# Performance work log

Hardware: AMD Instinct MI355X
Metric: run time of the kernel (lower is better)

Reference implementation:

```python
import jax, jax.numpy as jnp
import numpy as np
import math

EPS = 1.1920929e-07  # torch F.rms_norm default eps = fp32 machine epsilon


def rms_norm(x):
    # normalize over last dim, no learned weight (matches F.rms_norm(x, (d,)))
    var = jnp.mean(jnp.square(x), axis=-1, keepdims=True)
    return x * jax.lax.rsqrt(var + EPS)


def rotary(x, cos, sin):
    # x: (B, T, H, D); cos/sin: (T, D) -> broadcast over B, H
    d2 = x.shape[-1] // 2
    x1, x2 = x[..., :d2], x[..., d2:]
    rot = jnp.concatenate([-x2, x1], axis=-1)  # rotate_half
    c = cos[None, :, None, :]
    s = sin[None, :, None, :]
    return x * c + rot * s


def setup_inputs() -> dict:
    key = jax.random.key(0)
    ks = jax.random.split(key, 5)
    B, T, C, H = 2, 2048, 1024, 16
    D = C // H
    x = jax.random.normal(ks[0], (B, T, C), dtype=jnp.float32)
    # real RoPE tables (theta=10000), duplicated across the two halves
    inv_freq = 1.0 / (10000.0 ** (np.arange(0, D, 2, dtype=np.float32) / D))
    pos = np.arange(T, dtype=np.float32)
    freqs = np.outer(pos, inv_freq)            # (T, D/2)
    emb = np.concatenate([freqs, freqs], -1)   # (T, D)
    cos = jnp.asarray(np.cos(emb), dtype=jnp.float32)
    sin = jnp.asarray(np.sin(emb), dtype=jnp.float32)
    sc_in = 1.0 / math.sqrt(C)
    W_attn = jax.random.normal(ks[1], (C, 3 * C), dtype=jnp.float32) * sc_in
    b_attn = jax.random.normal(ks[2], (3 * C,), dtype=jnp.float32) * 0.02
    W_proj = jax.random.normal(ks[3], (C, C), dtype=jnp.float32) * sc_in
    b_proj = jax.random.normal(ks[4], (C,), dtype=jnp.float32) * 0.02
    return {"x": x, "cos": cos, "sin": sin, "W_attn": W_attn, "b_attn": b_attn,
            "W_proj": W_proj, "b_proj": b_proj}


def reference(x, cos, sin, W_attn, b_attn, W_proj, b_proj):
    B, T, C = x.shape
    H = 16
    D = C // H
    qkv = x @ W_attn + b_attn                         # (B, T, 3C)
    qkv = qkv.reshape(B, T, 3, H, D)                  # 'b t (a h d) -> ...'
    q, k, v = qkv[:, :, 0], qkv[:, :, 1], qkv[:, :, 2]  # (B, T, H, D)
    q, k = rms_norm(q), rms_norm(k)
    q = rotary(q, cos, sin)
    k = rotary(k, cos, sin)
    # causal SDPA, scale = 1/sqrt(D)
    scale = 1.0 / math.sqrt(D)
    scores = jnp.einsum('bthd,bshd->bhts', q, k) * scale  # (B, H, T, T)
    causal = jnp.tril(jnp.ones((T, T), dtype=bool))
    scores = jnp.where(causal[None, None], scores, jnp.finfo(scores.dtype).min)
    attn = jax.nn.softmax(scores, axis=-1)
    y = jnp.einsum('bhts,bshd->bthd', attn, v)            # (B, T, H, D)
    y = y.reshape(B, T, C)
    return y @ W_proj + b_proj
```

## Files before the change

kernel.cpp:

```cpp
#include <hip/hip_runtime.h>
#include <math.h>

#define EPSV 1.1920929e-07f

typedef __attribute__((ext_vector_type(8))) short short8;
typedef __attribute__((ext_vector_type(4))) float f32x4;

__device__ __forceinline__ float bf2f(unsigned short u) {
    union { unsigned int i; float f; } c; c.i = ((unsigned int)u) << 16; return c.f;
}
__device__ __forceinline__ unsigned short f2bf(float f) {
    union { float f; unsigned int i; } c; c.f = f;
    unsigned int r = c.i + 0x7FFFu + ((c.i >> 16) & 1u);
    return (unsigned short)(r >> 16);
}
__device__ __forceinline__ unsigned int pack_bf16_ru(float a, float b) {
    union { float f; unsigned int i; } ca, cb; ca.f = a; cb.f = b;
    return __builtin_amdgcn_perm(cb.i + 0x8000u, ca.i + 0x8000u, 0x07060302u);
}
__device__ __forceinline__ void async_lds16(const unsigned short* g, unsigned short* l) {
    __builtin_amdgcn_global_load_lds(
        (const __attribute__((address_space(1))) unsigned int*)g,
        (__attribute__((address_space(3))) unsigned int*)l, 16, 0, 0);
}

__global__ __launch_bounds__(256) void prep_cast_transpose(
    const float* __restrict__ x, unsigned short* __restrict__ xb, int nCast,
    const float* __restrict__ Wa, unsigned short* __restrict__ Wat,
    const float* __restrict__ Wp, unsigned short* __restrict__ Wpt,
    const float* __restrict__ cosp, const float* __restrict__ sinp,
    float2* __restrict__ cs, int castBlocks)
{
    __shared__ float tile[32][33];
    const int bxg = blockIdx.x;
    if (bxg < castBlocks) {
        const int i = (bxg * 256 + threadIdx.x) * 4;
        if (i >= nCast) return;
        const float4 v = *(const float4*)&x[i];
        ushort4 o;
        o.x = f2bf(v.x); o.y = f2bf(v.y); o.z = f2bf(v.z); o.w = f2bf(v.w);
        *(ushort4*)&xb[i] = o;
        return;
    }
    if (bxg >= castBlocks + 4096) {
        const int i = (bxg - castBlocks - 4096) * 256 + threadIdx.x;
        const int tp = i >> 5, dp = i & 31;
        cs[i] = make_float2(cosp[tp * 64 + dp], sinp[tp * 64 + dp]);
        return;
    }
    const int r0 = bxg - castBlocks;
    int bx = r0 & 127;
    const int by = r0 >> 7;
    const float* W; unsigned short* Wt; int N;
    if (bx < 96) { W = Wa; Wt = Wat; N = 3072; }
    else         { W = Wp; Wt = Wpt; N = 1024; bx -= 96; }
    const int n0 = bx * 32, k0 = by * 32;
    const int r = threadIdx.x >> 3, c4 = (threadIdx.x & 7) * 4;
    const float4 v = *(const float4*)&W[(size_t)(k0 + r) * N + n0 + c4];
    tile[r][c4 + 0] = v.x; tile[r][c4 + 1] = v.y;
    tile[r][c4 + 2] = v.z; tile[r][c4 + 3] = v.w;
    __syncthreads();
    ushort4 o;
    o.x = f2bf(tile[c4 + 0][r]); o.y = f2bf(tile[c4 + 1][r]);
    o.z = f2bf(tile[c4 + 2][r]); o.w = f2bf(tile[c4 + 3][r]);
    *(ushort4*)&Wt[(size_t)(n0 + r) * 1024 + k0 + c4] = o;
}

__global__ __launch_bounds__(256) void gemm_qkv(
    const unsigned short* __restrict__ A,
    const unsigned short* __restrict__ Bt,
    const float* __restrict__ bias,
    unsigned short* __restrict__ qkv,
    unsigned short* __restrict__ vt,
    const float2* __restrict__ cs,
    int M, int K, int T)
{
    const int N = 3072;
    __shared__ __align__(16) unsigned short smem[17408];
    unsigned short* As0 = smem;
    unsigned short* As1 = smem + 4096;
    unsigned short* Bs0 = smem + 8192;
    unsigned short* Bs1 = smem + 12288;

    const int t    = threadIdx.x;
    const int lane = t & 63;
    const int wv   = t >> 6;
    const int wrow = (wv >> 1) * 64;
    const int wcol = (wv & 1) * 64;
    const int m0 = blockIdx.y * 128;
    const int n0 = blockIdx.x * 128;
    const int col  = lane & 15;
    const int quad = lane >> 4;

    const int srow = (wv << 5) + (lane >> 2);
    const int scol = (lane & 3) << 3;
    const unsigned short* a00 = A  + (size_t)(m0 + srow) * K + scol;
    const unsigned short* a10 = a00 + (size_t)16 * K;
    const unsigned short* a01 = a00 + 32;
    const unsigned short* a11 = a10 + 32;
    const unsigned short* b00 = Bt + (size_t)(n0 + srow) * K + scol;
    const unsigned short* b10 = b00 + (size_t)16 * K;
    const unsigned short* b01 = b00 + 32;
    const unsigned short* b11 = b10 + 32;
    unsigned short* al0 = &As0[srow * 32 + scol];
    unsigned short* al1 = &As0[(srow + 16) * 32 + scol];
    unsigned short* al2 = &As1[srow * 32 + scol];
    unsigned short* al3 = &As1[(srow + 16) * 32 + scol];
    unsigned short* bl0 = &Bs0[srow * 32 + scol];
    unsigned short* bl1 = &Bs0[(srow + 16) * 32 + scol];
    unsigned short* bl2 = &Bs1[srow * 32 + scol];
    unsigned short* bl3 = &Bs1[(srow + 16) * 32 + scol];

    f32x4 acc[4][4];
    #pragma unroll
    for (int i = 0; i < 4; ++i)
        #pragma unroll
        for (int j = 0; j < 4; ++j)
            acc[i][j] = (f32x4){0.f, 0.f, 0.f, 0.f};

    for (int k0 = 0; k0 < K; k0 += 64) {
        async_lds16(a00, al0);
        async_lds16(a10, al1);
        async_lds16(a01, al2);
        async_lds16(a11, al3);
        async_lds16(b00, bl0);
        async_lds16(b10, bl1);
        async_lds16(b01, bl2);
        async_lds16(b11, bl3);
        a00 += 64; a10 += 64; a01 += 64; a11 += 64;
        b00 += 64; b10 += 64; b01 += 64; b11 += 64;
        __syncthreads();
        short8 af[2][4], bf[2][4];
        #pragma unroll
        for (int mt = 0; mt < 4; ++mt) {
            af[0][mt] = *(const short8*)&As0[(wrow + mt * 16 + col) * 32 + (quad << 3)];
            af[1][mt] = *(const short8*)&As1[(wrow + mt * 16 + col) * 32 + (quad << 3)];
        }
        #pragma unroll
        for (int nt = 0; nt < 4; ++nt) {
            bf[0][nt] = *(const short8*)&Bs0[(wcol + nt * 16 + col) * 32 + (quad << 3)];
            bf[1][nt] = *(const short8*)&Bs1[(wcol + nt * 16 + col) * 32 + (quad << 3)];
        }
        #pragma unroll
        for (int ks = 0; ks < 2; ++ks)
            #pragma unroll
            for (int mt = 0; mt < 4; ++mt)
                #pragma unroll
                for (int nt = 0; nt < 4; ++nt)
                    acc[mt][nt] = __builtin_amdgcn_mfma_f32_16x16x32_bf16(
                        af[ks][mt], bf[ks][nt], acc[mt][nt], 0, 0, 0);
        __syncthreads();
    }

    #pragma unroll
    for (int nt = 0; nt < 4; ++nt) {
        const float bv = bias[n0 + wcol + nt * 16 + col];
        #pragma unroll
        for (int mt = 0; mt < 4; ++mt)
            #pragma unroll
            for (int r = 0; r < 4; ++r)
                acc[mt][nt][r] += bv;
    }

    const int b     = m0 / T;
    const int tpos0 = m0 - b * T;

    if (n0 < 2048) {
        const int n_lin = n0 + wcol;
        const float scale = (n_lin < 1024) ? 0.18033688011112042f : 1.0f;
        #pragma unroll
        for (int mt = 0; mt < 4; ++mt) {
            #pragma unroll
            for (int r = 0; r < 4; ++r) {
                float ss = acc[mt][0][r] * acc[mt][0][r]
                         + acc[mt][1][r] * acc[mt][1][r]
                         + acc[mt][2][r] * acc[mt][2][r]
                         + acc[mt][3][r] * acc[mt][3][r];
                ss += __shfl_xor(ss, 1, 64);
                ss += __shfl_xor(ss, 2, 64);
                ss += __shfl_xor(ss, 4, 64);
                ss += __shfl_xor(ss, 8, 64);
                const float rn = rsqrtf(ss * (1.0f / 64.0f) + EPSV) * scale;
                const int tpos = tpos0 + wrow + mt * 16 + (quad << 2) + r;
                const float2 c0 = cs[tpos * 32 + col];
                const float2 c1 = cs[tpos * 32 + 16 + col];
                const float o0 = (acc[mt][0][r] * c0.x - acc[mt][2][r] * c0.y) * rn;
                const float o1 = (acc[mt][1][r] * c1.x - acc[mt][3][r] * c1.y) * rn;
                const float o2 = (acc[mt][2][r] * c0.x + acc[mt][0][r] * c0.y) * rn;
                const float o3 = (acc[mt][3][r] * c1.x + acc[mt][1][r] * c1.y) * rn;
                const int m = m0 + wrow + mt * 16 + (quad << 2) + r;
                unsigned short* qr = qkv + (size_t)m * N + n_lin + col;
                qr[0]  = f2bf(o0);
                qr[16] = f2bf(o1);
                qr[32] = f2bf(o2);
                qr[48] = f2bf(o3);
            }
        }
    } else {
        unsigned short (*vtile)[136] = (unsigned short(*)[136])smem;
        __syncthreads();
        #pragma unroll
        for (int nt = 0; nt < 4; ++nt)
            #pragma unroll
            for (int mt = 0; mt < 4; ++mt)
                #pragma unroll
                for (int r = 0; r < 4; ++r)
                    vtile[wcol + nt * 16 + col][wrow + mt * 16 + (quad << 2) + r]
                        = f2bf(acc[mt][nt][r]);
        __syncthreads();
        const int td = t >> 4;
        const int mloc = (t & 15) << 3;
        const int h2base = (n0 - 2048) >> 6;
        #pragma unroll
        for (int i = 0; i < 8; ++i) {
            const int dl = td + i * 16;
            const short8 o = *(const short8*)&vtile[dl][mloc];
            const int h2 = h2base + (dl >> 6);
            const size_t row = ((size_t)(b * 16 + h2) << 6) + (dl & 63);
            *(short8*)&vt[row * T + tpos0 + mloc] = o;
        }
    }
}

__global__ __launch_bounds__(256) void gemm_bf16_n64(
    const unsigned short* __restrict__ A,
    const unsigned short* __restrict__ Bt,
    const float* __restrict__ bias,
    float* __restrict__ C,
    int M, int N, int K)
{
    __shared__ __align__(16) unsigned short smem[12288];
    const int t    = threadIdx.x;
    const int lane = t & 63;
    const int wv   = t >> 6;
    const int wrow = wv << 5;
    const int m0 = blockIdx.y * 128;
    const int n0 = blockIdx.x * 64;
    const int col  = lane & 15;
    const int quad = lane >> 4;

    const int srw = lane >> 2;
    const int sck = (lane & 3) << 3;
    const unsigned short* aP0 = A  + (size_t)(m0 + (wv << 4) + srw) * K + sck;
    const unsigned short* aP1 = aP0 + (size_t)64 * K;
    const unsigned short* bP0 = Bt + (size_t)(n0 + (wv << 4) + srw) * K + sck;
    const int stoff = (wv << 9) + (lane << 3);
    unsigned short* aD = smem + stoff;
    unsigned short* bD = smem + 8192 + stoff;

    f32x4 acc[2][4];
    #pragma unroll
    for (int i = 0; i < 2; ++i)
        #pragma unroll
        for (int j = 0; j < 4; ++j)
            acc[i][j] = (f32x4){0.f, 0.f, 0.f, 0.f};

    async_lds16(aP0, aD);  async_lds16(aP1, aD + 2048);
    async_lds16(bP0, bD);
    aP0 += 32; aP1 += 32; bP0 += 32;

    const int NK = K >> 5;
    for (int kt = 0; kt < NK; ++kt) {
        __syncthreads();
        if (kt + 1 < NK) {
            const int nbA = ((kt + 1) & 1) << 12;
            const int nbB = ((kt + 1) & 1) << 11;
            async_lds16(aP0, aD + nbA);  async_lds16(aP1, aD + nbA + 2048);
            async_lds16(bP0, bD + nbB);
            aP0 += 32; aP1 += 32; bP0 += 32;
        }
        const unsigned short* Ac = smem + ((kt & 1) << 12);
        const unsigned short* Bc = smem + 8192 + ((kt & 1) << 11);
        short8 af[2], bf[4];
        #pragma unroll
        for (int mt = 0; mt < 2; ++mt)
            af[mt] = *(const short8*)&Ac[(wrow + mt * 16 + col) * 32 + (quad << 3)];
        #pragma unroll
        for (int nt = 0; nt < 4; ++nt)
            bf[nt] = *(const short8*)&Bc[(nt * 16 + col) * 32 + (quad << 3)];
        #pragma unroll
        for (int mt = 0; mt < 2; ++mt)
            #pragma unroll
            for (int nt = 0; nt < 4; ++nt)
                acc[mt][nt] = __builtin_amdgcn_mfma_f32_16x16x32_bf16(
                    af[mt], bf[nt], acc[mt][nt], 0, 0, 0);
    }

    const int rowq = quad << 2;
    #pragma unroll
    for (int nt = 0; nt < 4; ++nt) {
        const int n = n0 + nt * 16 + col;
        const float bv = bias[n];
        #pragma unroll
        for (int mt = 0; mt < 2; ++mt) {
            #pragma unroll
            for (int r = 0; r < 4; ++r) {
                const int m = m0 + wrow + mt * 16 + rowq + r;
                C[(size_t)m * N + n] = acc[mt][nt][r] + bv;
            }
        }
    }
}

__global__ __launch_bounds__(512, 4) void flash_attn_mfma(
    const unsigned short* __restrict__ qkv,
    const unsigned short* __restrict__ vt,
    unsigned short* __restrict__ yb,
    int B, int T)
{
    const int bh = blockIdx.x;
    const int b  = bh >> 4, h = bh & 15;
    const int ny = (int)gridDim.y;
    const int y  = (int)blockIdx.y;
    const int hny = (ny + 1) >> 1;
    const int jq = (y < hny) ? (ny - 1 - y) : (y - hny);
    const int q0 = jq << 7;
    const int t  = threadIdx.x;
    const int lane = t & 63;
    const int w    = t >> 6;
    const int col  = lane & 15;
    const int quad = lane >> 4;

    __shared__ __align__(16) unsigned short smem[25600];
    unsigned short* Kb = smem;
    unsigned short* Vb = smem + 8192;
    unsigned short* Ps = smem + 16384;

    const unsigned short* qb  = qkv + (size_t)b * T * 3072 + (h << 6);
    const unsigned short* kb  = qb + 1024;
    const unsigned short* vtb = vt + (size_t)bh * 64 * T;

    const int qw = q0 + (w << 4);
    const int qg = qw + col;

    short8 qf[2];
    {
        const unsigned short* qrow = qb + (size_t)qg * 3072 + (quad << 3);
        qf[0] = *(const short8*)&qrow[0];
        qf[1] = *(const short8*)&qrow[32];
    }

    f32x4 oacc[4];
    #pragma unroll
    for (int i = 0; i < 4; ++i) oacc[i] = (f32x4){0.f, 0.f, 0.f, 0.f};
    float l_i = 0.f;

    const int sr = t >> 3;
    const int sg = (((t & 7) ^ (sr & 7)) << 3);
    const unsigned short* kp = kb  + (size_t)sr * 3072 + sg;
    const unsigned short* vp = vtb + (size_t)sr * T + sg;

    async_lds16(kp, Kb + (t << 3));
    async_lds16(vp, Vb + (t << 3));
    kp += (size_t)64 * 3072; vp += 64;

    const int cs0 = ((quad ^ (col & 7)) << 3);
    const int cs1 = (((4 + quad) ^ (col & 7)) << 3);

    const int last_kt = (q0 + 127) >> 6;
    int cur = 0;
    for (int kt = 0; kt <= last_kt; ++kt) {
        const int k0 = kt << 6;
        __syncthreads();
        if (kt < last_kt) {
            async_lds16(kp, Kb + ((cur ^ 1) << 12) + (t << 3));
            async_lds16(vp, Vb + ((cur ^ 1) << 12) + (t << 3));
            kp += (size_t)64 * 3072; vp += 64;
        }

        if (k0 <= qw + 15) {
            const unsigned short* Kc = Kb + (cur << 12);
            const unsigned short* Vc = Vb + (cur << 12);

            f32x4 st[4];
            #pragma unroll
            for (int i = 0; i < 4; ++i) st[i] = (f32x4){0.f, 0.f, 0.f, 0.f};
            __builtin_amdgcn_s_setprio(1);
            #pragma unroll
            for (int ks = 0; ks < 2; ++ks)
                #pragma unroll
                for (int mt = 0; mt < 4; ++mt) {
                    const short8 kf = *(const short8*)&Kc[(mt * 16 + col) * 64 + (ks ? cs1 : cs0)];
                    st[mt] = __builtin_amdgcn_mfma_f32_16x16x32_bf16(kf, qf[ks], st[mt], 0, 0, 0);
                }
            __builtin_amdgcn_s_setprio(0);

            const bool diag = (k0 + 63 > qw);
            unsigned short* pw = Ps + ((w << 4) + col) * 72;
            float rs = 0.f;
            #pragma unroll
            for (int mt = 0; mt < 4; ++mt) {
                float x0 = st[mt][0], x1 = st[mt][1];
                float x2 = st[mt][2], x3 = st[mt][3];
                if (diag) {
                    const int sbase = k0 + mt * 16 + (quad << 2);
                    if (sbase + 0 > qg) x0 = -INFINITY;
                    if (sbase + 1 > qg) x1 = -INFINITY;
                    if (sbase + 2 > qg) x2 = -INFINITY;
                    if (sbase + 3 > qg) x3 = -INFINITY;
                }
                const float p0 = __builtin_amdgcn_exp2f(x0);
                const float p1 = __builtin_amdgcn_exp2f(x1);
                const float p2 = __builtin_amdgcn_exp2f(x2);
                const float p3 = __builtin_amdgcn_exp2f(x3);
                rs += (p0 + p1) + (p2 + p3);
                uint2 pk;
                pk.x = pack_bf16_ru(p0, p1);
                pk.y = pack_bf16_ru(p2, p3);
                *(uint2*)&pw[mt * 16 + (quad << 2)] = pk;
            }
            l_i += rs;

            __builtin_amdgcn_s_setprio(1);
            #pragma unroll
            for (int ks = 0; ks < 2; ++ks) {
                const short8 pf = *(const short8*)&Ps[((w << 4) + col) * 72 + ks * 32 + (quad << 3)];
                #pragma unroll
                for (int mt = 0; mt < 4; ++mt) {
                    const short8 vf = *(const short8*)&Vc[(mt * 16 + col) * 64 + (ks ? cs1 : cs0)];
                    oacc[mt] = __builtin_amdgcn_mfma_f32_16x16x32_bf16(vf, pf, oacc[mt], 0, 0, 0);
                }
            }
            __builtin_amdgcn_s_setprio(0);
        }
        cur ^= 1;
    }

    l_i += __shfl_xor(l_i, 16, 64);
    l_i += __shfl_xor(l_i, 32, 64);
    const float inv = 1.0f / l_i;
    unsigned short* yrow = yb + (size_t)(b * T + qg) * 1024 + (h << 6);
    #pragma unroll
    for (int mt = 0; mt < 4; ++mt) {
        ushort4 yv;
        yv.x = f2bf(oacc[mt][0] * inv);
        yv.y = f2bf(oacc[mt][1] * inv);
        yv.z = f2bf(oacc[mt][2] * inv);
        yv.w = f2bf(oacc[mt][3] * inv);
        *(ushort4*)&yrow[mt * 16 + (quad << 2)] = yv;
    }
}

extern "C" void kernel_launch(void* const* d_in, const int* in_sizes, int n_in,
                              void* d_out, int out_size, void* d_ws, size_t ws_size,
                              hipStream_t stream)
{
    const float* x      = (const float*)d_in[0];
    const float* cosp   = (const float*)d_in[1];
    const float* sinp   = (const float*)d_in[2];
    const float* W_attn = (const float*)d_in[3];
    const float* b_attn = (const float*)d_in[4];
    const float* W_proj = (const float*)d_in[5];
    const float* b_proj = (const float*)d_in[6];
    float* out = (float*)d_out;

    const int C = 1024, H = 16;
    const int T  = in_sizes[1] / 64;
    const int BT = in_sizes[0] / C;
    const int B  = BT / T;

    float2* csb          = (float2*)d_ws;
    unsigned short* qkvb = (unsigned short*)(csb + (size_t)T * 32);
    unsigned short* xb   = qkvb + (size_t)BT * 3072;
    unsigned short* Wab  = xb   + (size_t)BT * 1024;
    unsigned short* Wpb  = Wab  + (size_t)3072 * 1024;
    unsigned short* yb   = Wpb  + (size_t)1024 * 1024;
    unsigned short* vtb  = yb   + (size_t)BT * 1024;

    const int castBlocks = BT * C / 1024;
    const int csBlocks   = T * 32 / 256;
    prep_cast_transpose<<<dim3(castBlocks + 4096 + csBlocks), dim3(256), 0, stream>>>(
        x, xb, BT * C, W_attn, Wab, W_proj, Wpb, cosp, sinp, csb, castBlocks);

    gemm_qkv<<<dim3(3 * C / 128, BT / 128), dim3(256), 0, stream>>>(
        xb, Wab, b_attn, qkvb, vtb, csb, BT, C, T);

    flash_attn_mfma<<<dim3(B * H, T / 128), dim3(512), 0, stream>>>(
        qkvb, vtb, yb, B, T);

    gemm_bf16_n64<<<dim3(C / 64, BT / 128), dim3(256), 0, stream>>>(
        yb, Wpb, b_proj, out, BT, C, C);
}
```

Baseline: 174.6 us.

## Fuse x fp32-to-bf16 cast into QKV GEMM A-tile loading

The separate cast pass that turned x into a bf16 buffer is removed from the prep kernel. The QKV GEMM now streams fp32 x tiles straight into LDS, using an XOR swizzle to avoid bank conflicts, and converts them to bf16 when building MFMA fragments. This saves the bf16 x write and re-read. In exchange, A-tile global traffic per GEMM block doubles (fp32 instead of bf16), LDS use grows, and every block repeats the conversion for its A tile. Rounding changes from round-to-nearest-even to a simpler add-and-truncate.

```diff
diff --git a/kernel.cpp b/kernel.cpp
--- a/kernel.cpp
+++ b/kernel.cpp
@@ -18,39 +18,28 @@
     union { float f; unsigned int i; } ca, cb; ca.f = a; cb.f = b;
     return __builtin_amdgcn_perm(cb.i + 0x8000u, ca.i + 0x8000u, 0x07060302u);
 }
-__device__ __forceinline__ void async_lds16(const unsigned short* g, unsigned short* l) {
+__device__ __forceinline__ void async_lds16(const void* g, unsigned short* l) {
     __builtin_amdgcn_global_load_lds(
         (const __attribute__((address_space(1))) unsigned int*)g,
         (__attribute__((address_space(3))) unsigned int*)l, 16, 0, 0);
 }
 
 __global__ __launch_bounds__(256) void prep_cast_transpose(
-    const float* __restrict__ x, unsigned short* __restrict__ xb, int nCast,
     const float* __restrict__ Wa, unsigned short* __restrict__ Wat,
     const float* __restrict__ Wp, unsigned short* __restrict__ Wpt,
     const float* __restrict__ cosp, const float* __restrict__ sinp,
-    float2* __restrict__ cs, int castBlocks)
+    float2* __restrict__ cs)
 {
     __shared__ float tile[32][33];
     const int bxg = blockIdx.x;
-    if (bxg < castBlocks) {
-        const int i = (bxg * 256 + threadIdx.x) * 4;
-        if (i >= nCast) return;
-        const float4 v = *(const float4*)&x[i];
-        ushort4 o;
-        o.x = f2bf(v.x); o.y = f2bf(v.y); o.z = f2bf(v.z); o.w = f2bf(v.w);
-        *(ushort4*)&xb[i] = o;
-        return;
-    }
-    if (bxg >= castBlocks + 4096) {
-        const int i = (bxg - castBlocks - 4096) * 256 + threadIdx.x;
+    if (bxg >= 4096) {
+        const int i = (bxg - 4096) * 256 + threadIdx.x;
         const int tp = i >> 5, dp = i & 31;
         cs[i] = make_float2(cosp[tp * 64 + dp], sinp[tp * 64 + dp]);
         return;
     }
-    const int r0 = bxg - castBlocks;
-    int bx = r0 & 127;
-    const int by = r0 >> 7;
+    int bx = bxg & 127;
+    const int by = bxg >> 7;
     const float* W; unsigned short* Wt; int N;
     if (bx < 96) { W = Wa; Wt = Wat; N = 3072; }
     else         { W = Wp; Wt = Wpt; N = 1024; bx -= 96; }
@@ -67,7 +56,7 @@
 }
 
 __global__ __launch_bounds__(256) void gemm_qkv(
-    const unsigned short* __restrict__ A,
+    const float* __restrict__ X,
     const unsigned short* __restrict__ Bt,
     const float* __restrict__ bias,
     unsigned short* __restrict__ qkv,
@@ -76,11 +65,10 @@
     int M, int K, int T)
 {
     const int N = 3072;
-    __shared__ __align__(16) unsigned short smem[17408];
-    unsigned short* As0 = smem;
-    unsigned short* As1 = smem + 4096;
-    unsigned short* Bs0 = smem + 8192;
-    unsigned short* Bs1 = smem + 12288;
+    __shared__ __align__(16) unsigned short smem[24576];
+    float* Asf = (float*)smem;
+    unsigned short* Bs0 = smem + 16384;
+    unsigned short* Bs1 = smem + 20480;
 
     const int t    = threadIdx.x;
     const int lane = t & 63;
@@ -92,20 +80,16 @@
     const int col  = lane & 15;
     const int quad = lane >> 4;
 
+    const int aw = (wv << 2) + quad;
+    const float* xsrc = X + (size_t)(m0 + aw) * K + ((col ^ aw) << 2);
+    unsigned short* adst = smem + (((wv << 6) + lane) << 3);
+
     const int srow = (wv << 5) + (lane >> 2);
     const int scol = (lane & 3) << 3;
-    const unsigned short* a00 = A  + (size_t)(m0 + srow) * K + scol;
-    const unsigned short* a10 = a00 + (size_t)16 * K;
-    const unsigned short* a01 = a00 + 32;
-    const unsigned short* a11 = a10 + 32;
     const unsigned short* b00 = Bt + (size_t)(n0 + srow) * K + scol;
     const unsigned short* b10 = b00 + (size_t)16 * K;
     const unsigned short* b01 = b00 + 32;
     const unsigned short* b11 = b10 + 32;
-    unsigned short* al0 = &As0[srow * 32 + scol];
-    unsigned short* al1 = &As0[(srow + 16) * 32 + scol];
-    unsigned short* al2 = &As1[srow * 32 + scol];
-    unsigned short* al3 = &As1[(srow + 16) * 32 + scol];
     unsigned short* bl0 = &Bs0[srow * 32 + scol];
     unsigned short* bl1 = &Bs0[(srow + 16) * 32 + scol];
     unsigned short* bl2 = &Bs1[srow * 32 + scol];
@@ -118,23 +102,46 @@
         for (int j = 0; j < 4; ++j)
             acc[i][j] = (f32x4){0.f, 0.f, 0.f, 0.f};
 
+    const int ca0 = ((quad << 1) + 0) ^ col;
+    const int ca1 = ((quad << 1) + 1) ^ col;
+    const int cb0 = (8 + (quad << 1) + 0) ^ col;
+    const int cb1 = (8 + (quad << 1) + 1) ^ col;
+
     for (int k0 = 0; k0 < K; k0 += 64) {
-        async_lds16(a00, al0);
-        async_lds16(a10, al1);
-        async_lds16(a01, al2);
-        async_lds16(a11, al3);
+        #pragma unroll
+        for (int a = 0; a < 8; ++a)
+            async_lds16(xsrc + a * 16 * K, adst + (a << 11));
         async_lds16(b00, bl0);
         async_lds16(b10, bl1);
         async_lds16(b01, bl2);
         async_lds16(b11, bl3);
-        a00 += 64; a10 += 64; a01 += 64; a11 += 64;
+        xsrc += 64;
         b00 += 64; b10 += 64; b01 += 64; b11 += 64;
         __syncthreads();
+
         short8 af[2][4], bf[2][4];
         #pragma unroll
         for (int mt = 0; mt < 4; ++mt) {
-            af[0][mt] = *(const short8*)&As0[(wrow + mt * 16 + col) * 32 + (quad << 3)];
-            af[1][mt] = *(const short8*)&As1[(wrow + mt * 16 + col) * 32 + (quad << 3)];
+            const int ar = (wrow + mt * 16 + col) << 6;
+            union { short8 s; unsigned int u[4]; } c0, c1;
+            {
+                const f32x4 lo = *(const f32x4*)&Asf[ar + (ca0 << 2)];
+                const f32x4 hi = *(const f32x4*)&Asf[ar + (ca1 << 2)];
+                c0.u[0] = pack_bf16_ru(lo[0], lo[1]);
+                c0.u[1] = pack_bf16_ru(lo[2], lo[3]);
+                c0.u[2] = pack_bf16_ru(hi[0], hi[1]);
+                c0.u[3] = pack_bf16_ru(hi[2], hi[3]);
+            }
+            {
+                const f32x4 lo = *(const f32x4*)&Asf[ar + (cb0 << 2)];
+                const f32x4 hi = *(const f32x4*)&Asf[ar + (cb1 << 2)];
+                c1.u[0] = pack_bf16_ru(lo[0], lo[1]);
+                c1.u[1] = pack_bf16_ru(lo[2], lo[3]);
+                c1.u[2] = pack_bf16_ru(hi[0], hi[1]);
+                c1.u[3] = pack_bf16_ru(hi[2], hi[3]);
+            }
+            af[0][mt] = c0.s;
+            af[1][mt] = c1.s;
         }
         #pragma unroll
         for (int nt = 0; nt < 4; ++nt) {
@@ -461,19 +468,17 @@
 
     float2* csb          = (float2*)d_ws;
     unsigned short* qkvb = (unsigned short*)(csb + (size_t)T * 32);
-    unsigned short* xb   = qkvb + (size_t)BT * 3072;
-    unsigned short* Wab  = xb   + (size_t)BT * 1024;
+    unsigned short* Wab  = qkvb + (size_t)BT * 3072;
     unsigned short* Wpb  = Wab  + (size_t)3072 * 1024;
     unsigned short* yb   = Wpb  + (size_t)1024 * 1024;
     unsigned short* vtb  = yb   + (size_t)BT * 1024;
 
-    const int castBlocks = BT * C / 1024;
-    const int csBlocks   = T * 32 / 256;
-    prep_cast_transpose<<<dim3(castBlocks + 4096 + csBlocks), dim3(256), 0, stream>>>(
-        x, xb, BT * C, W_attn, Wab, W_proj, Wpb, cosp, sinp, csb, castBlocks);
+    const int csBlocks = T * 32 / 256;
+    prep_cast_transpose<<<dim3(4096 + csBlocks), dim3(256), 0, stream>>>(
+        W_attn, Wab, W_proj, Wpb, cosp, sinp, csb);
 
     gemm_qkv<<<dim3(3 * C / 128, BT / 128), dim3(256), 0, stream>>>(
-        xb, Wab, b_attn, qkvb, vtb, csb, BT, C, T);
+        x, Wab, b_attn, qkvb, vtb, csb, BT, C, T);
 
     flash_attn_mfma<<<dim3(B * H, T / 128), dim3(512), 0, stream>>>(
         qkvb, vtb, yb, B, T);
```

Measured after the change: 176.6 us. About the same (+1.2%).
